# Kernel optimization log

Hardware: AMD Instinct MI355X
Metric: run time of the kernel (lower is better)

Reference implementation:

```python
import jax, jax.numpy as jnp
import numpy as np

B, L, D = 4, 2048, 1024
E, K, FF = 8, 2, 4096
CAP_FACTOR = 1.25


def setup_inputs() -> dict:
    key = jax.random.key(0)
    ks = jax.random.split(key, 10)
    s = 0.02
    x = jax.random.normal(ks[0], (B, L, D), dtype=jnp.float32)
    noise = jax.random.normal(ks[1], (B, L, E), dtype=jnp.float32)
    Wg = jax.random.normal(ks[2], (D, E), dtype=jnp.float32) * s
    bg = jnp.zeros((E,), jnp.float32)
    Wn = jax.random.normal(ks[3], (D, E), dtype=jnp.float32) * s
    bn = jnp.zeros((E,), jnp.float32)
    W1 = jax.random.normal(ks[4], (E, D, FF), dtype=jnp.float32) * s
    b1 = jnp.zeros((E, FF), jnp.float32)
    W2 = jax.random.normal(ks[5], (E, FF, D), dtype=jnp.float32) * s
    b2 = jnp.zeros((E, D), jnp.float32)
    return {"x": x, "noise": noise, "Wg": Wg, "bg": bg, "Wn": Wn, "bn": bn,
            "W1": W1, "b1": b1, "W2": W2, "b2": b2}


def reference(x, noise, Wg, bg, Wn, bn, W1, b1, W2, b2):
    Bs, Ls, Ds = x.shape
    F_tot = Bs * Ls
    capacity = int(F_tot * K / E * CAP_FACTOR)

    # --- NoisyTopkRouter ---
    logits = jnp.einsum('bld,de->ble', x, Wg) + bg           # [B,L,E]
    noise_logits = jnp.einsum('bld,de->ble', x, Wn) + bn      # [B,L,E]
    noisy = logits + noise * jax.nn.softplus(noise_logits)
    topv, topi = jax.lax.top_k(noisy, K)                      # [B,L,K]
    # softmax over -inf-masked logits == softmax over the top-k values scattered back
    gates_k = jax.nn.softmax(topv, axis=-1)                   # [B,L,K]

    flat_x = x.reshape(F_tot, Ds)
    flat_idx = topi.reshape(F_tot, K)
    flat_gates = jnp.zeros((F_tot, E), x.dtype).at[
        jnp.arange(F_tot)[:, None], flat_idx].set(gates_k.reshape(F_tot, K))

    # --- capacity-aware dispatch (first `capacity` tokens in flat order, as torch nonzero[:capacity]) ---
    mask_EF = (flat_idx[None, :, :] == jnp.arange(E)[:, None, None]).any(-1)  # [E,F]
    pos_EF = jnp.cumsum(mask_EF, axis=1) - 1                                    # slot within expert
    keep_EF = mask_EF & (pos_EF < capacity)

    def build(keep_row, pos_row):
        buf = jnp.full((capacity,), F_tot, dtype=jnp.int32)  # sentinel -> padded zero row
        return buf.at[jnp.where(keep_row, pos_row, capacity)].set(
            jnp.arange(F_tot, dtype=jnp.int32), mode='drop')

    dispatch = jax.vmap(build)(keep_EF, pos_EF)               # [E, capacity]

    x_pad = jnp.concatenate([flat_x, jnp.zeros((1, Ds), x.dtype)], axis=0)
    g_pad = jnp.concatenate([flat_gates, jnp.zeros((1, E), x.dtype)], axis=0)

    # --- grouped expert FFN (gelu = exact, matching torch nn.GELU) ---
    xin = x_pad[dispatch]                                     # [E,C,D]
    h = jax.nn.gelu(jnp.einsum('ecd,edf->ecf', xin, W1) + b1[:, None, :], approximate=False)
    out = jnp.einsum('ecf,efd->ecd', h, W2) + b2[:, None, :]  # [E,C,D]
    gate = g_pad[dispatch, jnp.arange(E)[:, None]]            # [E,C]
    weighted = out * gate[..., None]

    # --- scatter-combine ---
    updates = jnp.zeros((F_tot + 1, Ds), x.dtype).at[dispatch.reshape(-1)].add(
        weighted.reshape(-1, Ds))
    return updates[:F_tot].reshape(Bs, Ls, Ds)
```

## Files before the change

kernel.cpp:

```cpp
#include <hip/hip_runtime.h>
#include <stdint.h>

typedef __bf16 bf16x8 __attribute__((ext_vector_type(8)));
typedef float  f32x4  __attribute__((ext_vector_type(4)));

#define F_TOT 8192
#define DIM   1024
#define NEXP  8
#define FF    4096
#define CAP   2560

__device__ __forceinline__ float b2f(unsigned short u){
    union { unsigned int u; float f; } c; c.u = ((unsigned int)u) << 16; return c.f;
}
__device__ __forceinline__ unsigned short f2b(float f){
    union { float f; unsigned int u; } c; c.f = f;
    unsigned int r = c.u + 0x7FFFu + ((c.u >> 16) & 1u);
    return (unsigned short)(r >> 16);
}
__device__ __forceinline__ float ldIn(const void* p, size_t i, int isb){
    return isb ? b2f(((const unsigned short*)p)[i]) : ((const float*)p)[i];
}
__device__ __forceinline__ void gl_lds16(const unsigned short* g, unsigned short* l){
    __builtin_amdgcn_global_load_lds(
        (const __attribute__((address_space(1))) unsigned int*)(g),
        (__attribute__((address_space(3))) unsigned int*)(l),
        16, 0, 0);
}

__global__ void detect_kernel(const unsigned short* __restrict__ x, int* __restrict__ flag){
    __shared__ int cnt;
    if (threadIdx.x == 0) cnt = 0;
    __syncthreads();
    unsigned short s = x[threadIdx.x];
    int e = s & 0x7F80;
    if (e >= 0x3000 && e <= 0x4800) atomicAdd(&cnt, 1);
    __syncthreads();
    if (threadIdx.x == 0) flag[0] = (cnt >= 410) ? 1 : 0;
}

__global__ void gating_kernel(const void* __restrict__ x,
                              const void* __restrict__ Wg, const void* __restrict__ bg,
                              const void* __restrict__ Wn, const void* __restrict__ bn,
                              const int* __restrict__ flag,
                              float* __restrict__ logits, float* __restrict__ nlogits)
{
    int tid = blockIdx.x * blockDim.x + threadIdx.x;
    int t = tid >> 4, o = tid & 15;
    int col = o & 7;
    int isb = flag[0];
    const void* W = (o < 8) ? Wg : Wn;
    float acc = 0.f;
    if (isb){
        const unsigned short* xr = (const unsigned short*)x + (size_t)t * DIM;
        const unsigned short* w  = (const unsigned short*)W;
        #pragma unroll 8
        for (int d = 0; d < DIM; d++) acc = fmaf(b2f(xr[d]), b2f(w[d * 8 + col]), acc);
    } else {
        const float* xr = (const float*)x + (size_t)t * DIM;
        const float* w  = (const float*)W;
        #pragma unroll 8
        for (int d = 0; d < DIM; d++) acc = fmaf(xr[d], w[d * 8 + col], acc);
    }
    acc += ldIn((o < 8) ? bg : bn, col, isb);
    ((o < 8) ? logits : nlogits)[t * 8 + col] = acc;
}

__global__ void route_kernel(const float* __restrict__ logits,
                             const float* __restrict__ nlogits,
                             const void* __restrict__ noise,
                             const int* __restrict__ flag,
                             int* __restrict__ topi, float* __restrict__ gates)
{
    int t = blockIdx.x * blockDim.x + threadIdx.x;
    int isb = flag[0];
    float ny[8];
    #pragma unroll
    for (int e = 0; e < 8; e++){
        float nl = nlogits[t * 8 + e];
        float sp = fmaxf(nl, 0.f) + log1pf(expf(-fabsf(nl)));
        ny[e] = logits[t * 8 + e] + ldIn(noise, (size_t)t * 8 + e, isb) * sp;
    }
    int i0 = 0; float v0 = ny[0];
    #pragma unroll
    for (int e = 1; e < 8; e++) if (ny[e] > v0){ v0 = ny[e]; i0 = e; }
    int i1 = -1; float v1 = -3.4e38f;
    #pragma unroll
    for (int e = 0; e < 8; e++) if (e != i0 && ny[e] > v1){ v1 = ny[e]; i1 = e; }
    float e1 = expf(v1 - v0);
    float den = 1.f + e1;
    topi[t * 2]      = i0;  topi[t * 2 + 1] = i1;
    gates[t * 2]     = 1.f / den;
    gates[t * 2 + 1] = e1 / den;
}

__global__ __launch_bounds__(1024)
void scan_kernel(const int* __restrict__ topi,
                 int* __restrict__ dispatch, int* __restrict__ slotf)
{
    int e = blockIdx.x;
    int tid = threadIdx.x;
    for (int c = tid; c < CAP; c += 1024) dispatch[e * CAP + c] = F_TOT;
    int base = tid * 8;
    int kk[8]; int cnt = 0;
    #pragma unroll
    for (int j = 0; j < 8; j++){
        int t = base + j;
        int k = (topi[t * 2] == e) ? 0 : ((topi[t * 2 + 1] == e) ? 1 : -1);
        kk[j] = k; if (k >= 0) cnt++;
    }
    __shared__ int s[1024];
    s[tid] = cnt; __syncthreads();
    for (int off = 1; off < 1024; off <<= 1){
        int v = (tid >= off) ? s[tid - off] : 0;
        __syncthreads();
        s[tid] += v;
        __syncthreads();
    }
    int pos = s[tid] - cnt;
    #pragma unroll
    for (int j = 0; j < 8; j++){
        if (kk[j] >= 0){
            int t = base + j;
            if (pos < CAP){
                dispatch[e * CAP + pos] = t;
                slotf[t * 2 + kk[j]] = e * CAP + pos;
            } else {
                slotf[t * 2 + kk[j]] = -1;
            }
            pos++;
        }
    }
}

__global__ void convx_kernel(const void* __restrict__ x, const int* __restrict__ flag,
                             unsigned short* __restrict__ xb)
{
    size_t i = ((size_t)blockIdx.x * blockDim.x + threadIdx.x) * 8;
    if (flag[0]){
        ushort4 a = *(const ushort4*)((const unsigned short*)x + i);
        ushort4 b = *(const ushort4*)((const unsigned short*)x + i + 4);
        *(ushort4*)(xb + i) = a;  *(ushort4*)(xb + i + 4) = b;
    } else {
        float4 a = *(const float4*)((const float*)x + i);
        float4 b = *(const float4*)((const float*)x + i + 4);
        ushort4 lo, hi;
        lo.x = f2b(a.x); lo.y = f2b(a.y); lo.z = f2b(a.z); lo.w = f2b(a.w);
        hi.x = f2b(b.x); hi.y = f2b(b.y); hi.z = f2b(b.z); hi.w = f2b(b.w);
        *(ushort4*)(xb + i) = lo; *(ushort4*)(xb + i + 4) = hi;
    }
}

__global__ void transpose_kernel(const void* __restrict__ in,
                                 unsigned short* __restrict__ out,
                                 const int* __restrict__ flag,
                                 int R, int C, int eBase)
{
    __shared__ unsigned short tile[64][68];
    const size_t mi = (size_t)(eBase + blockIdx.z) * R * C;
    const size_t mo = (size_t)blockIdx.z * R * C;
    int c0 = blockIdx.x * 64, r0 = blockIdx.y * 64;
    int t = threadIdx.x;
    int rr = t >> 4, cc = (t & 15) * 4;
    int isb = flag[0];
    #pragma unroll
    for (int i = 0; i < 4; i++){
        int r = rr + i * 16;
        size_t idx = mi + (size_t)(r0 + r) * C + c0 + cc;
        if (isb){
            ushort4 v = *(const ushort4*)((const unsigned short*)in + idx);
            *(ushort4*)&tile[r][cc] = v;
        } else {
            float4 v = *(const float4*)((const float*)in + idx);
            ushort4 u; u.x = f2b(v.x); u.y = f2b(v.y); u.z = f2b(v.z); u.w = f2b(v.w);
            *(ushort4*)&tile[r][cc] = u;
        }
    }
    __syncthreads();
    #pragma unroll
    for (int i = 0; i < 4; i++){
        int c = rr + i * 16;
        ushort4 v;
        v.x = tile[cc + 0][c]; v.y = tile[cc + 1][c];
        v.z = tile[cc + 2][c]; v.w = tile[cc + 3][c];
        *(ushort4*)(out + mo + (size_t)(c0 + c) * R + r0 + cc) = v;
    }
}

__global__ __launch_bounds__(256, 2)
void ffn0_kernel(const unsigned short* __restrict__ xb,
                 const unsigned short* __restrict__ Wt,
                 const void* __restrict__ b1,
                 const int* __restrict__ flag,
                 unsigned short* __restrict__ h,
                 const int* __restrict__ dispatch, int eBase)
{
    constexpr int KT = DIM, NT = FF, NTILES = NT / 128;
    const int el = blockIdx.y, eg = el + eBase;
    const int nt = blockIdx.x % NTILES;
    const int mt = blockIdx.x / NTILES;
    const int m0 = mt * 128, n0 = nt * 128;
    const int tid = threadIdx.x, lane = tid & 63, wave = tid >> 6;
    const int wm = wave >> 1, wn = wave & 1;
    const int quad = lane >> 4, l16 = lane & 15;

    __shared__ __align__(16) unsigned short As[128 * 32];
    __shared__ __align__(16) unsigned short Bs[128 * 32];

    const int r0 = tid >> 2, c8 = (tid & 3) * 8;
    int t0 = dispatch[eg * CAP + m0 + r0];
    int t1 = dispatch[eg * CAP + m0 + 64 + r0];
    bool v0 = ((unsigned)t0) < (unsigned)F_TOT;
    bool v1 = ((unsigned)t1) < (unsigned)F_TOT;
    const unsigned short* aS0 = xb + (v0 ? (size_t)t0 * DIM : 0) + c8;
    const unsigned short* aS1 = xb + (v1 ? (size_t)t1 * DIM : 0) + c8;
    const unsigned short* bE  = Wt + (size_t)el * NT * KT;
    const unsigned short* bS0 = bE + (size_t)(n0 + r0) * KT + c8;
    const unsigned short* bS1 = bE + (size_t)(n0 + 64 + r0) * KT + c8;

    f32x4 acc[4][4] = {};

    for (int k0 = 0; k0 < KT; k0 += 32){
        __syncthreads();
        gl_lds16(aS0, &As[tid * 8]);
        gl_lds16(aS1, &As[2048 + tid * 8]);
        gl_lds16(bS0, &Bs[tid * 8]);
        gl_lds16(bS1, &Bs[2048 + tid * 8]);
        aS0 += 32; aS1 += 32; bS0 += 32; bS1 += 32;
        __syncthreads();

        bf16x8 af[4], bfv[4];
        #pragma unroll
        for (int i = 0; i < 4; i++)
            af[i] = *(const bf16x8*)&As[(wm * 64 + i * 16 + l16) * 32 + quad * 8];
        #pragma unroll
        for (int j = 0; j < 4; j++)
            bfv[j] = *(const bf16x8*)&Bs[(wn * 64 + j * 16 + l16) * 32 + quad * 8];
        #pragma unroll
        for (int i = 0; i < 4; i++)
            #pragma unroll
            for (int j = 0; j < 4; j++)
                acc[i][j] = __builtin_amdgcn_mfma_f32_16x16x32_bf16(af[i], bfv[j], acc[i][j], 0, 0, 0);
    }

    const int isb = flag[0];
    const int rB = m0 + wm * 64 + quad * 4;
    const int cB = n0 + wn * 64 + l16;
    float bv[4];
    #pragma unroll
    for (int j = 0; j < 4; j++) bv[j] = ldIn(b1, (size_t)eg * NT + cB + j * 16, isb);
    #pragma unroll
    for (int i = 0; i < 4; i++)
        #pragma unroll
        for (int j = 0; j < 4; j++)
            #pragma unroll
            for (int r = 0; r < 4; r++){
                int row = rB + i * 16 + r;
                float v = acc[i][j][r] + bv[j];
                v = 0.5f * v * (1.0f + erff(v * 0.70710678118654752f));
                h[((size_t)(el * CAP + row)) * FF + cB + j * 16] = f2b(v);
            }
}

__global__ __launch_bounds__(256, 2)
void ffn1_kernel(const unsigned short* __restrict__ h,
                 const unsigned short* __restrict__ Wt,
                 const void* __restrict__ b2,
                 const int* __restrict__ flag,
                 unsigned short* __restrict__ eo,
                 int eBase)
{
    constexpr int KT = FF, NT = DIM, NTILES = NT / 128;
    const int el = blockIdx.y, eg = el + eBase;
    const int nt = blockIdx.x % NTILES;
    const int mt = blockIdx.x / NTILES;
    const int m0 = mt * 128, n0 = nt * 128;
    const int tid = threadIdx.x, lane = tid & 63, wave = tid >> 6;
    const int wm = wave >> 1, wn = wave & 1;
    const int quad = lane >> 4, l16 = lane & 15;

    __shared__ __align__(16) unsigned short As[128 * 32];
    __shared__ __align__(16) unsigned short Bs[128 * 32];

    const int r0 = tid >> 2, c8 = (tid & 3) * 8;
    const unsigned short* aS0 = h + ((size_t)(el * CAP + m0 + r0)) * KT + c8;
    const unsigned short* aS1 = h + ((size_t)(el * CAP + m0 + 64 + r0)) * KT + c8;
    const unsigned short* bE  = Wt + (size_t)el * NT * KT;
    const unsigned short* bS0 = bE + (size_t)(n0 + r0) * KT + c8;
    const unsigned short* bS1 = bE + (size_t)(n0 + 64 + r0) * KT + c8;

    f32x4 acc[4][4] = {};

    for (int k0 = 0; k0 < KT; k0 += 32){
        __syncthreads();
        gl_lds16(aS0, &As[tid * 8]);
        gl_lds16(aS1, &As[2048 + tid * 8]);
        gl_lds16(bS0, &Bs[tid * 8]);
        gl_lds16(bS1, &Bs[2048 + tid * 8]);
        aS0 += 32; aS1 += 32; bS0 += 32; bS1 += 32;
        __syncthreads();

        bf16x8 af[4], bfv[4];
        #pragma unroll
        for (int i = 0; i < 4; i++)
            af[i] = *(const bf16x8*)&As[(wm * 64 + i * 16 + l16) * 32 + quad * 8];
        #pragma unroll
        for (int j = 0; j < 4; j++)
            bfv[j] = *(const bf16x8*)&Bs[(wn * 64 + j * 16 + l16) * 32 + quad * 8];
        #pragma unroll
        for (int i = 0; i < 4; i++)
            #pragma unroll
            for (int j = 0; j < 4; j++)
                acc[i][j] = __builtin_amdgcn_mfma_f32_16x16x32_bf16(af[i], bfv[j], acc[i][j], 0, 0, 0);
    }

    const int isb = flag[0];
    const int rB = m0 + wm * 64 + quad * 4;
    const int cB = n0 + wn * 64 + l16;
    float bv[4];
    #pragma unroll
    for (int j = 0; j < 4; j++) bv[j] = ldIn(b2, (size_t)eg * NT + cB + j * 16, isb);
    #pragma unroll
    for (int i = 0; i < 4; i++)
        #pragma unroll
        for (int j = 0; j < 4; j++)
            #pragma unroll
            for (int r = 0; r < 4; r++){
                int row = rB + i * 16 + r;
                eo[((size_t)(eg * CAP + row)) * DIM + cB + j * 16] = f2b(acc[i][j][r] + bv[j]);
            }
}

__global__ void combine_kernel(const unsigned short* __restrict__ eo,
                               const int* __restrict__ slotf,
                               const float* __restrict__ gates,
                               const int* __restrict__ flag,
                               void* __restrict__ out)
{
    int t = blockIdx.x;
    int d = threadIdx.x * 4;
    int s0 = slotf[t * 2], s1 = slotf[t * 2 + 1];
    float g0 = gates[t * 2], g1 = gates[t * 2 + 1];
    float a0 = 0.f, a1 = 0.f, a2 = 0.f, a3 = 0.f;
    if (((unsigned)s0) < (unsigned)(NEXP * CAP)){
        ushort4 a = *(const ushort4*)(eo + (size_t)s0 * DIM + d);
        a0 += g0 * b2f(a.x); a1 += g0 * b2f(a.y);
        a2 += g0 * b2f(a.z); a3 += g0 * b2f(a.w);
    }
    if (((unsigned)s1) < (unsigned)(NEXP * CAP)){
        ushort4 a = *(const ushort4*)(eo + (size_t)s1 * DIM + d);
        a0 += g1 * b2f(a.x); a1 += g1 * b2f(a.y);
        a2 += g1 * b2f(a.z); a3 += g1 * b2f(a.w);
    }
    if (flag[0]){
        ushort4 o; o.x = f2b(a0); o.y = f2b(a1); o.z = f2b(a2); o.w = f2b(a3);
        *(ushort4*)((unsigned short*)out + (size_t)t * DIM + d) = o;
    } else {
        float4 o; o.x = a0; o.y = a1; o.z = a2; o.w = a3;
        *(float4*)((float*)out + (size_t)t * DIM + d) = o;
    }
}

extern "C" void kernel_launch(void* const* d_in, const int* in_sizes, int n_in,
                              void* d_out, int out_size, void* d_ws, size_t ws_size,
                              hipStream_t stream)
{
    const void* x     = d_in[0];
    const void* noise = d_in[1];
    const void* Wg    = d_in[2];
    const void* bg    = d_in[3];
    const void* Wn    = d_in[4];
    const void* bn    = d_in[5];
    const void* W1    = d_in[6];
    const void* b1    = d_in[7];
    const void* W2    = d_in[8];
    const void* b2    = d_in[9];
    char* ws = (char*)d_ws;

    float* logits  = (float*)(ws + 0);
    float* nlogits = (float*)(ws + 262144);
    int*   topi    = (int*)  (ws + 524288);
    float* gates   = (float*)(ws + 589824);
    int*   disp    = (int*)  (ws + 655360);
    int*   slotf   = (int*)  (ws + 737280);
    int*   flag    = (int*)  (ws + 802816);
    unsigned short* xb = (unsigned short*)(ws + 1048576);
    unsigned short* Wt = (unsigned short*)(ws + 17825792);
    unsigned short* h  = (unsigned short*)(ws + 51380224);
    unsigned short* eo = (unsigned short*)(ws + 135266304);

    detect_kernel<<<1, 512, 0, stream>>>((const unsigned short*)x, flag);
    gating_kernel<<<512, 256, 0, stream>>>(x, Wg, bg, Wn, bn, flag, logits, nlogits);
    route_kernel<<<32, 256, 0, stream>>>(logits, nlogits, noise, flag, topi, gates);
    scan_kernel<<<8, 1024, 0, stream>>>(topi, disp, slotf);
    convx_kernel<<<4096, 256, 0, stream>>>(x, flag, xb);

    for (int g = 0; g < 2; g++){
        int eB = g * 4;
        transpose_kernel<<<dim3(64, 16, 4), 256, 0, stream>>>(W1, Wt, flag, DIM, FF, eB);
        ffn0_kernel<<<dim3((FF/128) * (CAP/128), 4), 256, 0, stream>>>(
            xb, Wt, b1, flag, h, disp, eB);
        transpose_kernel<<<dim3(16, 64, 4), 256, 0, stream>>>(W2, Wt, flag, FF, DIM, eB);
        ffn1_kernel<<<dim3((DIM/128) * (CAP/128), 4), 256, 0, stream>>>(
            h, Wt, b2, flag, eo, eB);
    }
    combine_kernel<<<F_TOT, 256, 0, stream>>>(eo, slotf, gates, flag, d_out);
}
```

Before: 911.9 us.

## Replace expert FFN GEMMs with 256x256 multi-stage pipelined kernel and skip empty tiles

Merges the two expert GEMM kernels into one templated kernel. It uses 256x256 tiles with 8 waves, a 4-deep LDS ring fed by async global-to-LDS loads with vmcnt waits, XOR-swizzled LDS reads to avoid bank conflicts, and setprio around MFMA bursts. The scan kernel now writes per-expert token counts so blocks whose row range lies past the expert's fill are skipped. The aim is to hide load latency behind the matrix math and stop computing padded capacity rows. In exchange it uses 128KB of LDS per block and more register pressure from the 8x4 accumulator array, which may limit occupancy.

```diff
diff --git a/kernel.cpp b/kernel.cpp
--- a/kernel.cpp
+++ b/kernel.cpp
@@ -26,6 +26,12 @@
         (const __attribute__((address_space(1))) unsigned int*)(g),
         (__attribute__((address_space(3))) unsigned int*)(l),
         16, 0, 0);
+}
+
+template<int W> __device__ __forceinline__ void waitcnt_vm(){
+    if constexpr (W == 8)      asm volatile("s_waitcnt vmcnt(8)" ::: "memory");
+    else if constexpr (W == 4) asm volatile("s_waitcnt vmcnt(4)" ::: "memory");
+    else                       asm volatile("s_waitcnt vmcnt(0)" ::: "memory");
 }
 
 __global__ void detect_kernel(const unsigned short* __restrict__ x, int* __restrict__ flag){
@@ -96,7 +102,8 @@
 
 __global__ __launch_bounds__(1024)
 void scan_kernel(const int* __restrict__ topi,
-                 int* __restrict__ dispatch, int* __restrict__ slotf)
+                 int* __restrict__ dispatch, int* __restrict__ slotf,
+                 int* __restrict__ cntbuf)
 {
     int e = blockIdx.x;
     int tid = threadIdx.x;
@@ -117,6 +124,7 @@
         s[tid] += v;
         __syncthreads();
     }
+    if (tid == 1023) cntbuf[e] = s[1023];
     int pos = s[tid] - cnt;
     #pragma unroll
     for (int j = 0; j < 8; j++){
@@ -187,147 +195,139 @@
     }
 }
 
-__global__ __launch_bounds__(256, 2)
-void ffn0_kernel(const unsigned short* __restrict__ xb,
-                 const unsigned short* __restrict__ Wt,
-                 const void* __restrict__ b1,
-                 const int* __restrict__ flag,
-                 unsigned short* __restrict__ h,
-                 const int* __restrict__ dispatch, int eBase)
-{
-    constexpr int KT = DIM, NT = FF, NTILES = NT / 128;
+
+#define STAGE_A(kt) { \
+    unsigned short* d_ = smem + (((kt)&3)<<14) + (tid<<3); \
+    gl_lds16(aS0 + (size_t)(kt)*32, d_); \
+    gl_lds16(aS1 + (size_t)(kt)*32, d_ + 4096); }
+
+#define STAGE_B(kt) { \
+    unsigned short* d_ = smem + (((kt)&3)<<14) + 8192 + (tid<<3); \
+    gl_lds16(bS0 + (size_t)(kt)*32, d_); \
+    gl_lds16(bS1 + (size_t)(kt)*32, d_ + 4096); }
+
+#define KTILE(T, DS, W) { \
+    waitcnt_vm<W>(); \
+    __builtin_amdgcn_s_barrier(); \
+    asm volatile("" ::: "memory"); \
+    const char* bufc = (const char*)smem + (((size_t)((T)&3))<<15); \
+    bf16x8 bfv[4], afv[4]; \
+    _Pragma("unroll") \
+    for (int j = 0; j < 4; j++){ \
+        int r_ = rB0 + j*16 + l16; \
+        bfv[j] = *(const bf16x8*)(bufc + boff + (((r_<<6)|(quad<<4)) ^ sx)); \
+    } \
+    _Pragma("unroll") \
+    for (int i = 0; i < 4; i++){ \
+        int r_ = i*16 + l16; \
+        afv[i] = *(const bf16x8*)(bufc + aoff + (((r_<<6)|(quad<<4)) ^ sx)); \
+    } \
+    if (DS){ STAGE_A((T)+3); } \
+    __builtin_amdgcn_s_setprio(1); \
+    _Pragma("unroll") \
+    for (int i = 0; i < 4; i++) \
+        _Pragma("unroll") \
+        for (int j = 0; j < 4; j++) \
+            acc[i][j] = __builtin_amdgcn_mfma_f32_16x16x32_bf16(afv[i], bfv[j], acc[i][j], 0, 0, 0); \
+    __builtin_amdgcn_s_setprio(0); \
+    __builtin_amdgcn_s_barrier(); \
+    _Pragma("unroll") \
+    for (int i = 0; i < 4; i++){ \
+        int r_ = (i+4)*16 + l16; \
+        afv[i] = *(const bf16x8*)(bufc + aoff + (((r_<<6)|(quad<<4)) ^ sx)); \
+    } \
+    if (DS){ STAGE_B((T)+3); } \
+    __builtin_amdgcn_s_setprio(1); \
+    _Pragma("unroll") \
+    for (int i = 0; i < 4; i++) \
+        _Pragma("unroll") \
+        for (int j = 0; j < 4; j++) \
+            acc[i+4][j] = __builtin_amdgcn_mfma_f32_16x16x32_bf16(afv[i], bfv[j], acc[i+4][j], 0, 0, 0); \
+    __builtin_amdgcn_s_setprio(0); \
+}
+
+template<int KT, int NT, bool ISF0>
+__global__ __launch_bounds__(512, 2)
+void ffn_pipe_kernel(const unsigned short* __restrict__ Ain,
+                     const unsigned short* __restrict__ Wt,
+                     const void* __restrict__ bias,
+                     const int* __restrict__ flag,
+                     unsigned short* __restrict__ Out,
+                     const int* __restrict__ dispatch,
+                     const int* __restrict__ cnt,
+                     int eBase)
+{
+    constexpr int NTN = NT / 256;
+    constexpr int NK  = KT / 32;
     const int el = blockIdx.y, eg = el + eBase;
-    const int nt = blockIdx.x % NTILES;
-    const int mt = blockIdx.x / NTILES;
-    const int m0 = mt * 128, n0 = nt * 128;
+    const int nt = blockIdx.x % NTN;
+    const int mt = blockIdx.x / NTN;
+    const int m0 = mt * 256, n0 = nt * 256;
+    if (m0 >= cnt[eg]) return;
+
     const int tid = threadIdx.x, lane = tid & 63, wave = tid >> 6;
-    const int wm = wave >> 1, wn = wave & 1;
+    const int wm = wave >> 2, wn = wave & 3;
     const int quad = lane >> 4, l16 = lane & 15;
-
-    __shared__ __align__(16) unsigned short As[128 * 32];
-    __shared__ __align__(16) unsigned short Bs[128 * 32];
-
-    const int r0 = tid >> 2, c8 = (tid & 3) * 8;
-    int t0 = dispatch[eg * CAP + m0 + r0];
-    int t1 = dispatch[eg * CAP + m0 + 64 + r0];
-    bool v0 = ((unsigned)t0) < (unsigned)F_TOT;
-    bool v1 = ((unsigned)t1) < (unsigned)F_TOT;
-    const unsigned short* aS0 = xb + (v0 ? (size_t)t0 * DIM : 0) + c8;
-    const unsigned short* aS1 = xb + (v1 ? (size_t)t1 * DIM : 0) + c8;
+    const int sx = (l16 & 7) << 4;
+    const int aoff = wm * 8192;
+    const int boff = 16384 + (wn >> 1) * 8192;
+    const int rB0  = (wn & 1) * 64;
+
+    __shared__ __align__(16) unsigned short smem[65536];
+
+    const int P  = tid;
+    const int q2 = ((P >> 2) ^ (P >> 4)) & 1;
+    const int q1 = ((P >> 1) ^ (P >> 3)) & 1;
+    const int q0 = (P ^ (P >> 2) ^ (P >> 4)) & 1;
+    const int L  = (P & ~7) | (q2 << 2) | (q1 << 1) | q0;
+    const int rs = L >> 2;
+    const int cs = (L & 3) * 8;
+
+    const unsigned short* aS0;
+    const unsigned short* aS1;
+    if (ISF0){
+        int t0 = dispatch[eg * CAP + m0 + rs];
+        int t1 = dispatch[eg * CAP + m0 + 128 + rs];
+        if (((unsigned)t0) >= (unsigned)F_TOT) t0 = 0;
+        if (((unsigned)t1) >= (unsigned)F_TOT) t1 = 0;
+        aS0 = Ain + (size_t)t0 * KT + cs;
+        aS1 = Ain + (size_t)t1 * KT + cs;
+    } else {
+        aS0 = Ain + ((size_t)(el * CAP + m0 + rs)) * KT + cs;
+        aS1 = Ain + ((size_t)(el * CAP + m0 + 128 + rs)) * KT + cs;
+    }
     const unsigned short* bE  = Wt + (size_t)el * NT * KT;
-    const unsigned short* bS0 = bE + (size_t)(n0 + r0) * KT + c8;
-    const unsigned short* bS1 = bE + (size_t)(n0 + 64 + r0) * KT + c8;
-
-    f32x4 acc[4][4] = {};
-
-    for (int k0 = 0; k0 < KT; k0 += 32){
-        __syncthreads();
-        gl_lds16(aS0, &As[tid * 8]);
-        gl_lds16(aS1, &As[2048 + tid * 8]);
-        gl_lds16(bS0, &Bs[tid * 8]);
-        gl_lds16(bS1, &Bs[2048 + tid * 8]);
-        aS0 += 32; aS1 += 32; bS0 += 32; bS1 += 32;
-        __syncthreads();
-
-        bf16x8 af[4], bfv[4];
-        #pragma unroll
-        for (int i = 0; i < 4; i++)
-            af[i] = *(const bf16x8*)&As[(wm * 64 + i * 16 + l16) * 32 + quad * 8];
-        #pragma unroll
-        for (int j = 0; j < 4; j++)
-            bfv[j] = *(const bf16x8*)&Bs[(wn * 64 + j * 16 + l16) * 32 + quad * 8];
-        #pragma unroll
-        for (int i = 0; i < 4; i++)
-            #pragma unroll
-            for (int j = 0; j < 4; j++)
-                acc[i][j] = __builtin_amdgcn_mfma_f32_16x16x32_bf16(af[i], bfv[j], acc[i][j], 0, 0, 0);
-    }
+    const unsigned short* bS0 = bE + (size_t)(n0 + rs) * KT + cs;
+    const unsigned short* bS1 = bE + (size_t)(n0 + 128 + rs) * KT + cs;
+
+    f32x4 acc[8][4] = {};
+
+    STAGE_A(0); STAGE_B(0);
+    STAGE_A(1); STAGE_B(1);
+    STAGE_A(2); STAGE_B(2);
+
+    for (int t = 0; t < NK - 3; ++t){ KTILE(t, 1, 8); }
+    KTILE(NK - 3, 0, 8);
+    KTILE(NK - 2, 0, 4);
+    KTILE(NK - 1, 0, 0);
 
     const int isb = flag[0];
-    const int rB = m0 + wm * 64 + quad * 4;
-    const int cB = n0 + wn * 64 + l16;
+    const int rBase = m0 + wm * 128 + quad * 4;
+    const int cBase = n0 + wn * 64 + l16;
     float bv[4];
     #pragma unroll
-    for (int j = 0; j < 4; j++) bv[j] = ldIn(b1, (size_t)eg * NT + cB + j * 16, isb);
-    #pragma unroll
-    for (int i = 0; i < 4; i++)
+    for (int j = 0; j < 4; j++) bv[j] = ldIn(bias, (size_t)eg * NT + cBase + j * 16, isb);
+    const int oe = ISF0 ? el : eg;
+    #pragma unroll
+    for (int i = 0; i < 8; i++)
         #pragma unroll
         for (int j = 0; j < 4; j++)
             #pragma unroll
             for (int r = 0; r < 4; r++){
-                int row = rB + i * 16 + r;
+                int row = rBase + i * 16 + r;
                 float v = acc[i][j][r] + bv[j];
-                v = 0.5f * v * (1.0f + erff(v * 0.70710678118654752f));
-                h[((size_t)(el * CAP + row)) * FF + cB + j * 16] = f2b(v);
-            }
-}
-
-__global__ __launch_bounds__(256, 2)
-void ffn1_kernel(const unsigned short* __restrict__ h,
-                 const unsigned short* __restrict__ Wt,
-                 const void* __restrict__ b2,
-                 const int* __restrict__ flag,
-                 unsigned short* __restrict__ eo,
-                 int eBase)
-{
-    constexpr int KT = FF, NT = DIM, NTILES = NT / 128;
-    const int el = blockIdx.y, eg = el + eBase;
-    const int nt = blockIdx.x % NTILES;
-    const int mt = blockIdx.x / NTILES;
-    const int m0 = mt * 128, n0 = nt * 128;
-    const int tid = threadIdx.x, lane = tid & 63, wave = tid >> 6;
-    const int wm = wave >> 1, wn = wave & 1;
-    const int quad = lane >> 4, l16 = lane & 15;
-
-    __shared__ __align__(16) unsigned short As[128 * 32];
-    __shared__ __align__(16) unsigned short Bs[128 * 32];
-
-    const int r0 = tid >> 2, c8 = (tid & 3) * 8;
-    const unsigned short* aS0 = h + ((size_t)(el * CAP + m0 + r0)) * KT + c8;
-    const unsigned short* aS1 = h + ((size_t)(el * CAP + m0 + 64 + r0)) * KT + c8;
-    const unsigned short* bE  = Wt + (size_t)el * NT * KT;
-    const unsigned short* bS0 = bE + (size_t)(n0 + r0) * KT + c8;
-    const unsigned short* bS1 = bE + (size_t)(n0 + 64 + r0) * KT + c8;
-
-    f32x4 acc[4][4] = {};
-
-    for (int k0 = 0; k0 < KT; k0 += 32){
-        __syncthreads();
-        gl_lds16(aS0, &As[tid * 8]);
-        gl_lds16(aS1, &As[2048 + tid * 8]);
-        gl_lds16(bS0, &Bs[tid * 8]);
-        gl_lds16(bS1, &Bs[2048 + tid * 8]);
-        aS0 += 32; aS1 += 32; bS0 += 32; bS1 += 32;
-        __syncthreads();
-
-        bf16x8 af[4], bfv[4];
-        #pragma unroll
-        for (int i = 0; i < 4; i++)
-            af[i] = *(const bf16x8*)&As[(wm * 64 + i * 16 + l16) * 32 + quad * 8];
-        #pragma unroll
-        for (int j = 0; j < 4; j++)
-            bfv[j] = *(const bf16x8*)&Bs[(wn * 64 + j * 16 + l16) * 32 + quad * 8];
-        #pragma unroll
-        for (int i = 0; i < 4; i++)
-            #pragma unroll
-            for (int j = 0; j < 4; j++)
-                acc[i][j] = __builtin_amdgcn_mfma_f32_16x16x32_bf16(af[i], bfv[j], acc[i][j], 0, 0, 0);
-    }
-
-    const int isb = flag[0];
-    const int rB = m0 + wm * 64 + quad * 4;
-    const int cB = n0 + wn * 64 + l16;
-    float bv[4];
-    #pragma unroll
-    for (int j = 0; j < 4; j++) bv[j] = ldIn(b2, (size_t)eg * NT + cB + j * 16, isb);
-    #pragma unroll
-    for (int i = 0; i < 4; i++)
-        #pragma unroll
-        for (int j = 0; j < 4; j++)
-            #pragma unroll
-            for (int r = 0; r < 4; r++){
-                int row = rB + i * 16 + r;
-                eo[((size_t)(eg * CAP + row)) * DIM + cB + j * 16] = f2b(acc[i][j][r] + bv[j]);
+                if (ISF0) v = 0.5f * v * (1.0f + erff(v * 0.70710678118654752f));
+                Out[((size_t)(oe * CAP + row)) * NT + cBase + j * 16] = f2b(v);
             }
 }
 
@@ -384,6 +384,7 @@
     int*   disp    = (int*)  (ws + 655360);
     int*   slotf   = (int*)  (ws + 737280);
     int*   flag    = (int*)  (ws + 802816);
+    int*   cnt     = (int*)  (ws + 803072);
     unsigned short* xb = (unsigned short*)(ws + 1048576);
     unsigned short* Wt = (unsigned short*)(ws + 17825792);
     unsigned short* h  = (unsigned short*)(ws + 51380224);
@@ -392,17 +393,17 @@
     detect_kernel<<<1, 512, 0, stream>>>((const unsigned short*)x, flag);
     gating_kernel<<<512, 256, 0, stream>>>(x, Wg, bg, Wn, bn, flag, logits, nlogits);
     route_kernel<<<32, 256, 0, stream>>>(logits, nlogits, noise, flag, topi, gates);
-    scan_kernel<<<8, 1024, 0, stream>>>(topi, disp, slotf);
+    scan_kernel<<<8, 1024, 0, stream>>>(topi, disp, slotf, cnt);
     convx_kernel<<<4096, 256, 0, stream>>>(x, flag, xb);
 
     for (int g = 0; g < 2; g++){
         int eB = g * 4;
         transpose_kernel<<<dim3(64, 16, 4), 256, 0, stream>>>(W1, Wt, flag, DIM, FF, eB);
-        ffn0_kernel<<<dim3((FF/128) * (CAP/128), 4), 256, 0, stream>>>(
-            xb, Wt, b1, flag, h, disp, eB);
+        ffn_pipe_kernel<DIM, FF, true><<<dim3((FF/256) * (CAP/256), 4), 512, 0, stream>>>(
+            xb, Wt, b1, flag, h, disp, cnt, eB);
         transpose_kernel<<<dim3(16, 64, 4), 256, 0, stream>>>(W2, Wt, flag, FF, DIM, eB);
-        ffn1_kernel<<<dim3((DIM/128) * (CAP/128), 4), 256, 0, stream>>>(
-            h, Wt, b2, flag, eo, eB);
+        ffn_pipe_kernel<FF, DIM, false><<<dim3((DIM/256) * (CAP/256), 4), 512, 0, stream>>>(
+            h, Wt, b2, flag, eo, disp, cnt, eB);
     }
     combine_kernel<<<F_TOT, 256, 0, stream>>>(eo, slotf, gates, flag, d_out);
 }
```

New measurement: 892.9 us. 1.02x faster.

## Fuse routing prologue kernels and skip empty expert row tiles in FFN

Applied to the files above, without the earlier changes.

Detection, gating, top-2 routing and x-to-bf16 conversion are merged into one kernel, and the logits stay in shared memory instead of going through global buffers. The scan kernel records each expert's clamped token count. Both FFN GEMM kernels exit early for 128-row tiles beyond that count, avoiding compute on padded capacity rows. The trade-offs are redundant per-block format detection and leaving the padded h/eo rows unwritten.

```diff
diff --git a/kernel.cpp b/kernel.cpp
--- a/kernel.cpp
+++ b/kernel.cpp
@@ -28,75 +28,118 @@
         16, 0, 0);
 }
 
-__global__ void detect_kernel(const unsigned short* __restrict__ x, int* __restrict__ flag){
-    __shared__ int cnt;
-    if (threadIdx.x == 0) cnt = 0;
+__global__ __launch_bounds__(256)
+void gating_kernel(const void* __restrict__ x,
+                   const void* __restrict__ noise,
+                   const void* __restrict__ Wg, const void* __restrict__ bg,
+                   const void* __restrict__ Wn, const void* __restrict__ bn,
+                   int* __restrict__ flag,
+                   int* __restrict__ topi, float* __restrict__ gates,
+                   unsigned short* __restrict__ xb)
+{
+    __shared__ int sflag;
+    __shared__ float lg[16][17];
+    const int g = blockIdx.x, tid = threadIdx.x;
+    const unsigned short* xs = (const unsigned short*)x;
+
+    if (tid == 0) sflag = 0;
     __syncthreads();
-    unsigned short s = x[threadIdx.x];
-    int e = s & 0x7F80;
-    if (e >= 0x3000 && e <= 0x4800) atomicAdd(&cnt, 1);
+    {
+        int c = 0;
+        unsigned short s0 = xs[tid], s1 = xs[tid + 256];
+        int e0 = s0 & 0x7F80, e1 = s1 & 0x7F80;
+        if (e0 >= 0x3000 && e0 <= 0x4800) c++;
+        if (e1 >= 0x3000 && e1 <= 0x4800) c++;
+        if (c) atomicAdd(&sflag, c);
+    }
     __syncthreads();
-    if (threadIdx.x == 0) flag[0] = (cnt >= 410) ? 1 : 0;
-}
-
-__global__ void gating_kernel(const void* __restrict__ x,
-                              const void* __restrict__ Wg, const void* __restrict__ bg,
-                              const void* __restrict__ Wn, const void* __restrict__ bn,
-                              const int* __restrict__ flag,
-                              float* __restrict__ logits, float* __restrict__ nlogits)
-{
-    int tid = blockIdx.x * blockDim.x + threadIdx.x;
-    int t = tid >> 4, o = tid & 15;
-    int col = o & 7;
-    int isb = flag[0];
+    const int isb = (sflag >= 410) ? 1 : 0;
+    if (g == 0 && tid == 0) flag[0] = isb;
+
+    const int tl = tid >> 4, o = tid & 15, col = o & 7;
+    const int t = g * 16 + tl;
     const void* W = (o < 8) ? Wg : Wn;
     float acc = 0.f;
     if (isb){
-        const unsigned short* xr = (const unsigned short*)x + (size_t)t * DIM;
+        const unsigned short* xr = xs + (size_t)t * DIM;
         const unsigned short* w  = (const unsigned short*)W;
-        #pragma unroll 8
-        for (int d = 0; d < DIM; d++) acc = fmaf(b2f(xr[d]), b2f(w[d * 8 + col]), acc);
+        for (int d = 0; d < DIM; d += 8){
+            ushort4 a = *(const ushort4*)(xr + d);
+            ushort4 b = *(const ushort4*)(xr + d + 4);
+            acc = fmaf(b2f(a.x), b2f(w[(d+0)*8+col]), acc);
+            acc = fmaf(b2f(a.y), b2f(w[(d+1)*8+col]), acc);
+            acc = fmaf(b2f(a.z), b2f(w[(d+2)*8+col]), acc);
+            acc = fmaf(b2f(a.w), b2f(w[(d+3)*8+col]), acc);
+            acc = fmaf(b2f(b.x), b2f(w[(d+4)*8+col]), acc);
+            acc = fmaf(b2f(b.y), b2f(w[(d+5)*8+col]), acc);
+            acc = fmaf(b2f(b.z), b2f(w[(d+6)*8+col]), acc);
+            acc = fmaf(b2f(b.w), b2f(w[(d+7)*8+col]), acc);
+        }
     } else {
         const float* xr = (const float*)x + (size_t)t * DIM;
         const float* w  = (const float*)W;
-        #pragma unroll 8
-        for (int d = 0; d < DIM; d++) acc = fmaf(xr[d], w[d * 8 + col], acc);
+        for (int d = 0; d < DIM; d += 8){
+            float4 a = *(const float4*)(xr + d);
+            float4 b = *(const float4*)(xr + d + 4);
+            acc = fmaf(a.x, w[(d+0)*8+col], acc);
+            acc = fmaf(a.y, w[(d+1)*8+col], acc);
+            acc = fmaf(a.z, w[(d+2)*8+col], acc);
+            acc = fmaf(a.w, w[(d+3)*8+col], acc);
+            acc = fmaf(b.x, w[(d+4)*8+col], acc);
+            acc = fmaf(b.y, w[(d+5)*8+col], acc);
+            acc = fmaf(b.z, w[(d+6)*8+col], acc);
+            acc = fmaf(b.w, w[(d+7)*8+col], acc);
+        }
     }
     acc += ldIn((o < 8) ? bg : bn, col, isb);
-    ((o < 8) ? logits : nlogits)[t * 8 + col] = acc;
-}
-
-__global__ void route_kernel(const float* __restrict__ logits,
-                             const float* __restrict__ nlogits,
-                             const void* __restrict__ noise,
-                             const int* __restrict__ flag,
-                             int* __restrict__ topi, float* __restrict__ gates)
-{
-    int t = blockIdx.x * blockDim.x + threadIdx.x;
-    int isb = flag[0];
-    float ny[8];
-    #pragma unroll
-    for (int e = 0; e < 8; e++){
-        float nl = nlogits[t * 8 + e];
-        float sp = fmaxf(nl, 0.f) + log1pf(expf(-fabsf(nl)));
-        ny[e] = logits[t * 8 + e] + ldIn(noise, (size_t)t * 8 + e, isb) * sp;
-    }
-    int i0 = 0; float v0 = ny[0];
-    #pragma unroll
-    for (int e = 1; e < 8; e++) if (ny[e] > v0){ v0 = ny[e]; i0 = e; }
-    int i1 = -1; float v1 = -3.4e38f;
-    #pragma unroll
-    for (int e = 0; e < 8; e++) if (e != i0 && ny[e] > v1){ v1 = ny[e]; i1 = e; }
-    float e1 = expf(v1 - v0);
-    float den = 1.f + e1;
-    topi[t * 2]      = i0;  topi[t * 2 + 1] = i1;
-    gates[t * 2]     = 1.f / den;
-    gates[t * 2 + 1] = e1 / den;
+    lg[tl][o] = acc;
+    __syncthreads();
+
+    if (tid < 16){
+        const int tt = g * 16 + tid;
+        float ny[8];
+        #pragma unroll
+        for (int e = 0; e < 8; e++){
+            float nl = lg[tid][8 + e];
+            float sp = fmaxf(nl, 0.f) + log1pf(expf(-fabsf(nl)));
+            ny[e] = lg[tid][e] + ldIn(noise, (size_t)tt * 8 + e, isb) * sp;
+        }
+        int i0 = 0; float v0 = ny[0];
+        #pragma unroll
+        for (int e = 1; e < 8; e++) if (ny[e] > v0){ v0 = ny[e]; i0 = e; }
+        int i1 = -1; float v1 = -3.4e38f;
+        #pragma unroll
+        for (int e = 0; e < 8; e++) if (e != i0 && ny[e] > v1){ v1 = ny[e]; i1 = e; }
+        float e1 = expf(v1 - v0);
+        float den = 1.f + e1;
+        topi[tt * 2]      = i0;  topi[tt * 2 + 1] = i1;
+        gates[tt * 2]     = 1.f / den;
+        gates[tt * 2 + 1] = e1 / den;
+    }
+
+    const size_t base = (size_t)g * 16384;
+    #pragma unroll
+    for (int it = 0; it < 8; it++){
+        size_t i = base + (size_t)it * 2048 + tid * 8;
+        if (isb){
+            ushort4 a = *(const ushort4*)(xs + i);
+            ushort4 b = *(const ushort4*)(xs + i + 4);
+            *(ushort4*)(xb + i) = a;  *(ushort4*)(xb + i + 4) = b;
+        } else {
+            float4 a = *(const float4*)((const float*)x + i);
+            float4 b = *(const float4*)((const float*)x + i + 4);
+            ushort4 lo, hi;
+            lo.x = f2b(a.x); lo.y = f2b(a.y); lo.z = f2b(a.z); lo.w = f2b(a.w);
+            hi.x = f2b(b.x); hi.y = f2b(b.y); hi.z = f2b(b.z); hi.w = f2b(b.w);
+            *(ushort4*)(xb + i) = lo; *(ushort4*)(xb + i + 4) = hi;
+        }
+    }
 }
 
 __global__ __launch_bounds__(1024)
 void scan_kernel(const int* __restrict__ topi,
-                 int* __restrict__ dispatch, int* __restrict__ slotf)
+                 int* __restrict__ dispatch, int* __restrict__ slotf,
+                 int* __restrict__ cntbuf)
 {
     int e = blockIdx.x;
     int tid = threadIdx.x;
@@ -117,6 +160,7 @@
         s[tid] += v;
         __syncthreads();
     }
+    if (tid == 1023){ int tot = s[1023]; cntbuf[e] = tot > CAP ? CAP : tot; }
     int pos = s[tid] - cnt;
     #pragma unroll
     for (int j = 0; j < 8; j++){
@@ -133,24 +177,6 @@
     }
 }
 
-__global__ void convx_kernel(const void* __restrict__ x, const int* __restrict__ flag,
-                             unsigned short* __restrict__ xb)
-{
-    size_t i = ((size_t)blockIdx.x * blockDim.x + threadIdx.x) * 8;
-    if (flag[0]){
-        ushort4 a = *(const ushort4*)((const unsigned short*)x + i);
-        ushort4 b = *(const ushort4*)((const unsigned short*)x + i + 4);
-        *(ushort4*)(xb + i) = a;  *(ushort4*)(xb + i + 4) = b;
-    } else {
-        float4 a = *(const float4*)((const float*)x + i);
-        float4 b = *(const float4*)((const float*)x + i + 4);
-        ushort4 lo, hi;
-        lo.x = f2b(a.x); lo.y = f2b(a.y); lo.z = f2b(a.z); lo.w = f2b(a.w);
-        hi.x = f2b(b.x); hi.y = f2b(b.y); hi.z = f2b(b.z); hi.w = f2b(b.w);
-        *(ushort4*)(xb + i) = lo; *(ushort4*)(xb + i + 4) = hi;
-    }
-}
-
 __global__ void transpose_kernel(const void* __restrict__ in,
                                  unsigned short* __restrict__ out,
                                  const int* __restrict__ flag,
@@ -193,13 +219,15 @@
                  const void* __restrict__ b1,
                  const int* __restrict__ flag,
                  unsigned short* __restrict__ h,
-                 const int* __restrict__ dispatch, int eBase)
+                 const int* __restrict__ dispatch,
+                 const int* __restrict__ cnt, int eBase)
 {
     constexpr int KT = DIM, NT = FF, NTILES = NT / 128;
     const int el = blockIdx.y, eg = el + eBase;
     const int nt = blockIdx.x % NTILES;
     const int mt = blockIdx.x / NTILES;
     const int m0 = mt * 128, n0 = nt * 128;
+    if (m0 >= cnt[eg]) return;
     const int tid = threadIdx.x, lane = tid & 63, wave = tid >> 6;
     const int wm = wave >> 1, wn = wave & 1;
     const int quad = lane >> 4, l16 = lane & 15;
@@ -268,13 +296,14 @@
                  const void* __restrict__ b2,
                  const int* __restrict__ flag,
                  unsigned short* __restrict__ eo,
-                 int eBase)
+                 const int* __restrict__ cnt, int eBase)
 {
     constexpr int KT = FF, NT = DIM, NTILES = NT / 128;
     const int el = blockIdx.y, eg = el + eBase;
     const int nt = blockIdx.x % NTILES;
     const int mt = blockIdx.x / NTILES;
     const int m0 = mt * 128, n0 = nt * 128;
+    if (m0 >= cnt[eg]) return;
     const int tid = threadIdx.x, lane = tid & 63, wave = tid >> 6;
     const int wm = wave >> 1, wn = wave & 1;
     const int quad = lane >> 4, l16 = lane & 15;
@@ -377,32 +406,29 @@
     const void* b2    = d_in[9];
     char* ws = (char*)d_ws;
 
-    float* logits  = (float*)(ws + 0);
-    float* nlogits = (float*)(ws + 262144);
     int*   topi    = (int*)  (ws + 524288);
     float* gates   = (float*)(ws + 589824);
     int*   disp    = (int*)  (ws + 655360);
     int*   slotf   = (int*)  (ws + 737280);
     int*   flag    = (int*)  (ws + 802816);
+    int*   cnt     = (int*)  (ws + 803072);
     unsigned short* xb = (unsigned short*)(ws + 1048576);
     unsigned short* Wt = (unsigned short*)(ws + 17825792);
     unsigned short* h  = (unsigned short*)(ws + 51380224);
     unsigned short* eo = (unsigned short*)(ws + 135266304);
 
-    detect_kernel<<<1, 512, 0, stream>>>((const unsigned short*)x, flag);
-    gating_kernel<<<512, 256, 0, stream>>>(x, Wg, bg, Wn, bn, flag, logits, nlogits);
-    route_kernel<<<32, 256, 0, stream>>>(logits, nlogits, noise, flag, topi, gates);
-    scan_kernel<<<8, 1024, 0, stream>>>(topi, disp, slotf);
-    convx_kernel<<<4096, 256, 0, stream>>>(x, flag, xb);
+    gating_kernel<<<512, 256, 0, stream>>>(x, noise, Wg, bg, Wn, bn,
+                                           flag, topi, gates, xb);
+    scan_kernel<<<8, 1024, 0, stream>>>(topi, disp, slotf, cnt);
 
     for (int g = 0; g < 2; g++){
         int eB = g * 4;
         transpose_kernel<<<dim3(64, 16, 4), 256, 0, stream>>>(W1, Wt, flag, DIM, FF, eB);
         ffn0_kernel<<<dim3((FF/128) * (CAP/128), 4), 256, 0, stream>>>(
-            xb, Wt, b1, flag, h, disp, eB);
+            xb, Wt, b1, flag, h, disp, cnt, eB);
         transpose_kernel<<<dim3(16, 64, 4), 256, 0, stream>>>(W2, Wt, flag, FF, DIM, eB);
         ffn1_kernel<<<dim3((DIM/128) * (CAP/128), 4), 256, 0, stream>>>(
-            h, Wt, b2, flag, eo, eB);
+            h, Wt, b2, flag, eo, cnt, eB);
     }
     combine_kernel<<<F_TOT, 256, 0, stream>>>(eo, slotf, gates, flag, d_out);
 }
```

After: 853.8 us. 6.4% less time.
